# Optimization experiments

Hardware: AMD Instinct MI355X
Metric: run time of the kernel (lower is better)

Reference implementation:

```python
import jax, jax.numpy as jnp
import numpy as np

B, T, OBS = 256, 512, 256
H = 128          # OptimizedLSTMCell hidden size (hardcoded in module)
LATENT = 16


def setup_inputs() -> dict:
    key = jax.random.key(0)
    ks = jax.random.split(key, 6)
    xs = jax.random.normal(ks[0], (B, T, OBS), dtype=jnp.float32)
    # fused LSTM weights: gates ordered (i, f, g, o), each of width H
    Wx = jax.random.normal(ks[1], (OBS, 4 * H), dtype=jnp.float32) / np.sqrt(OBS)
    Wh = jax.random.normal(ks[2], (H, 4 * H), dtype=jnp.float32) / np.sqrt(H)
    b = jnp.zeros((4 * H,), dtype=jnp.float32)
    W1 = jax.random.normal(ks[3], (H, H), dtype=jnp.float32) / np.sqrt(H)
    b1 = jnp.zeros((H,), dtype=jnp.float32)
    W2 = jax.random.normal(ks[4], (H, 2 * LATENT), dtype=jnp.float32) / np.sqrt(H)
    b2 = jnp.zeros((2 * LATENT,), dtype=jnp.float32)
    return {"xs": xs, "Wx": Wx, "Wh": Wh, "b": b,
            "W1": W1, "b1": b1, "W2": W2, "b2": b2}


def reference(xs, Wx, Wh, b, W1, b1, W2, b2):
    # LSTM over time (flax OptimizedLSTMCell math, zero initial carry)
    bsz = xs.shape[0]
    hdim = Wh.shape[0]

    def step(carry, x_t):
        c, h = carry
        gates = x_t @ Wx + h @ Wh + b            # [B, 4H]
        i, f, g, o = jnp.split(gates, 4, axis=-1)
        i = jax.nn.sigmoid(i)
        f = jax.nn.sigmoid(f)
        g = jnp.tanh(g)
        o = jax.nn.sigmoid(o)
        c = f * c + i * g
        h = o * jnp.tanh(c)
        return (c, h), None

    init = (jnp.zeros((bsz, hdim), xs.dtype), jnp.zeros((bsz, hdim), xs.dtype))
    (_, h_last), _ = jax.lax.scan(step, init, jnp.swapaxes(xs, 0, 1))

    out = jax.nn.relu(h_last @ W1 + b1)          # [B, H]
    p = out @ W2 + b2                            # [B, 2*latent]
    mean, logvar = jnp.split(p, 2, axis=-1)
    return mean, logvar
```

## Files before the change

### kernel.cpp

```cpp
#include <hip/hip_runtime.h>
#include <hip/hip_fp16.h>

typedef unsigned short u16;
typedef unsigned int u32;

#define B_   256
#define T_   512
#define OBS_ 256
#define H_   128
#define G4_  512
#define LAT_ 16

typedef _Float16 half8_t __attribute__((ext_vector_type(8)));
typedef _Float16 half2_t __attribute__((ext_vector_type(2)));
typedef float    f32x4_t __attribute__((ext_vector_type(4)));

#if defined(__has_builtin)
#if __has_builtin(__builtin_amdgcn_fdot2)
#define HAVE_FDOT2 1
#endif
#endif

__device__ __forceinline__ u16 f2h(float x) { return __half_as_ushort(__float2half(x)); }
__device__ __forceinline__ float h2f(u16 u) { return __half2float(__ushort_as_half(u)); }
__device__ __forceinline__ float frcp(float x) { return __builtin_amdgcn_rcpf(x); }
__device__ __forceinline__ float fsigmoid(float x) { return frcp(1.f + __expf(-x)); }
__device__ __forceinline__ float ftanh(float x) { return 1.f - 2.f * frcp(1.f + __expf(2.f * x)); }

__device__ __forceinline__ float dot2acc(u32 w, u32 h, float acc) {
  half2_t wv = __builtin_bit_cast(half2_t, w);
  half2_t hv = __builtin_bit_cast(half2_t, h);
#ifdef HAVE_FDOT2
  return __builtin_amdgcn_fdot2(wv, hv, acc, false);
#else
  acc = fmaf((float)wv.x, (float)hv.x, acc);
  acc = fmaf((float)wv.y, (float)hv.y, acc);
  return acc;
#endif
}

__device__ __forceinline__ int permcol(int n) { return (n & 3) * 128 + (n >> 2); }

__global__ __launch_bounds__(256) void prep_kernel(const float* __restrict__ Wx,
                                                   const float* __restrict__ Wh,
                                                   const float* __restrict__ bias,
                                                   u16* __restrict__ Wxt,
                                                   u32* __restrict__ Whp,
                                                   float* __restrict__ biasp) {
  int idx = blockIdx.x * 256 + threadIdx.x;
  if (idx < G4_ * OBS_) {
    int n = idx / OBS_, k = idx % OBS_;
    Wxt[idx] = f2h(Wx[(size_t)k * G4_ + permcol(n)]);
  } else if (idx < G4_ * OBS_ + (H_ / 2) * G4_) {
    int i2 = idx - G4_ * OBS_;
    int k2 = i2 / G4_, n = i2 % G4_;
    int pn = permcol(n);
    u32 lo = f2h(Wh[(size_t)(2 * k2) * G4_ + pn]);
    u32 hi = f2h(Wh[(size_t)(2 * k2 + 1) * G4_ + pn]);
    Whp[i2] = lo | (hi << 16);
  } else if (idx < G4_ * OBS_ + (H_ / 2) * G4_ + G4_) {
    int n = idx - G4_ * OBS_ - (H_ / 2) * G4_;
    biasp[n] = bias[permcol(n)];
  }
}

__global__ __launch_bounds__(256, 2) void gemm_xw(const float* __restrict__ xs,
                                                  const u16* __restrict__ Wxt,
                                                  u16* __restrict__ Xw,
                                                  int t0, int ct_log2) {
  __shared__ __align__(16) u16 As[128][88];
  __shared__ __align__(16) u16 Bs[128][88];

  const int tid  = threadIdx.x;
  const int lane = tid & 63;
  const int w    = tid >> 6;
  const int qr   = (w & 1) * 64;
  const int qc   = (w >> 1) * 64;
  const int bn   = blockIdx.x;
  const int bm   = blockIdx.y;

  f32x4_t acc[4][4];
#pragma unroll
  for (int a = 0; a < 4; ++a)
#pragma unroll
    for (int bq = 0; bq < 4; ++bq)
      acc[a][bq] = (f32x4_t){0.f, 0.f, 0.f, 0.f};

  const int row  = tid >> 1;
  const int half = (tid & 1) * 32;
  const int m    = bm * 128 + row;
  const int bb   = m >> ct_log2;
  const int tau  = m & ((1 << ct_log2) - 1);
  const float* asrc = xs + (size_t)(bb * T_ + t0 + tau) * OBS_ + half;
  const u16*   bsrc = Wxt + (size_t)(bn * 128 + row) * OBS_ + half;

  for (int k0 = 0; k0 < OBS_; k0 += 64) {
    {
      const float* s = asrc + k0;
#pragma unroll
      for (int i = 0; i < 4; ++i) {
        float4 v0 = *(const float4*)(s + i * 8);
        float4 v1 = *(const float4*)(s + i * 8 + 4);
        uint4 pk;
        pk.x = (u32)f2h(v0.x) | ((u32)f2h(v0.y) << 16);
        pk.y = (u32)f2h(v0.z) | ((u32)f2h(v0.w) << 16);
        pk.z = (u32)f2h(v1.x) | ((u32)f2h(v1.y) << 16);
        pk.w = (u32)f2h(v1.z) | ((u32)f2h(v1.w) << 16);
        *(uint4*)&As[row][half + i * 8] = pk;
      }
    }
    {
      const u16* s = bsrc + k0;
#pragma unroll
      for (int i = 0; i < 4; ++i)
        *(uint4*)&Bs[row][half + i * 8] = *(const uint4*)(s + i * 8);
    }
    __syncthreads();
#pragma unroll
    for (int ks = 0; ks < 2; ++ks) {
      const int kc = ks * 32 + (lane >> 4) * 8;
      half8_t af[4], bf[4];
#pragma unroll
      for (int mi = 0; mi < 4; ++mi) af[mi] = *(const half8_t*)&As[qr + mi * 16 + (lane & 15)][kc];
#pragma unroll
      for (int ni = 0; ni < 4; ++ni) bf[ni] = *(const half8_t*)&Bs[qc + ni * 16 + (lane & 15)][kc];
#pragma unroll
      for (int mi = 0; mi < 4; ++mi)
#pragma unroll
        for (int ni = 0; ni < 4; ++ni)
          acc[mi][ni] = __builtin_amdgcn_mfma_f32_16x16x32_f16(af[mi], bf[ni], acc[mi][ni], 0, 0, 0);
    }
    __syncthreads();
  }
#pragma unroll
  for (int mi = 0; mi < 4; ++mi)
#pragma unroll
    for (int ni = 0; ni < 4; ++ni)
#pragma unroll
      for (int r = 0; r < 4; ++r) {
        int mm = bm * 128 + qr + mi * 16 + (lane >> 4) * 4 + r;
        int nn = bn * 128 + qc + ni * 16 + (lane & 15);
        Xw[(size_t)mm * G4_ + nn] = f2h(acc[mi][ni][r]);
      }
}

__global__ __launch_bounds__(512, 1) void lstm_rec(const u16* __restrict__ Xw,
                                                   const u32* __restrict__ Whp,
                                                   const float* __restrict__ biasp,
                                                   float* __restrict__ c_ws,
                                                   u16* __restrict__ h_ws,
                                                   int t0, int CT) {
  const int bb = blockIdx.x;
  const int tn = threadIdx.x;
  const int q  = tn & 3;
  const int j  = tn >> 2;
  __shared__ uint4 hq[2][16];

  u32 wh[64];
#pragma unroll
  for (int k2 = 0; k2 < 64; ++k2) wh[k2] = Whp[k2 * 512 + tn];
#pragma unroll
  for (int k2 = 0; k2 < 64; ++k2) asm volatile("" : "+v"(wh[k2]));
  const float bj = biasp[tn];

  float c = 0.f;
  if (t0 == 0) {
    if (tn < 32) ((uint4*)hq)[tn] = make_uint4(0u, 0u, 0u, 0u);
  } else {
    if (tn < 128) ((u16*)hq[0])[tn] = h_ws[bb * 128 + tn];
    if (q == 0) c = c_ws[bb * 128 + j];
  }
  __syncthreads();

  const u16* xwp = Xw + (size_t)bb * CT * 512 + tn;

  auto step = [&](u16 xcur, int cur) {
    float a0 = 0.f, a1 = 0.f, a2 = 0.f, a3 = 0.f;
#pragma unroll
    for (int qq = 0; qq < 16; ++qq) {
      uint4 hv = hq[cur][qq];
      a0 = dot2acc(wh[4 * qq + 0], hv.x, a0);
      a1 = dot2acc(wh[4 * qq + 1], hv.y, a1);
      a2 = dot2acc(wh[4 * qq + 2], hv.z, a2);
      a3 = dot2acc(wh[4 * qq + 3], hv.w, a3);
    }
    float pre = ((a0 + a1) + (a2 + a3)) + bj + h2f(xcur);
    float s1 = __shfl_xor(pre, 1);
    float s2 = __shfl_xor(pre, 2);
    float s3 = __shfl_xor(s1, 2);
    if (q == 0) {
      float ig = fsigmoid(pre);
      float fg = fsigmoid(s1);
      float gg = ftanh(s2);
      float og = fsigmoid(s3);
      c = fg * c + ig * gg;
      ((u16*)hq[cur ^ 1])[j] = f2h(og * ftanh(c));
    }
    __syncthreads();
  };

  u16 x0 = xwp[0 * 512], x1 = xwp[1 * 512], x2 = xwp[2 * 512], x3 = xwp[3 * 512];
  for (int t = 0; t < CT; t += 4) {
    u16 n0 = 0, n1 = 0, n2 = 0, n3 = 0;
    if (t + 4 < CT) {
      n0 = xwp[(size_t)(t + 4) * 512];
      n1 = xwp[(size_t)(t + 5) * 512];
      n2 = xwp[(size_t)(t + 6) * 512];
      n3 = xwp[(size_t)(t + 7) * 512];
    }
    step(x0, 0);
    step(x1, 1);
    step(x2, 0);
    step(x3, 1);
    x0 = n0; x1 = n1; x2 = n2; x3 = n3;
  }
  if (q == 0) {
    c_ws[bb * 128 + j] = c;
    h_ws[bb * 128 + j] = ((u16*)hq[0])[j];
  }
}

__global__ __launch_bounds__(128) void head_kernel(const u16* __restrict__ h_ws,
                                                   const float* __restrict__ W1,
                                                   const float* __restrict__ b1,
                                                   const float* __restrict__ W2,
                                                   const float* __restrict__ b2,
                                                   float* __restrict__ out) {
  const int bb = blockIdx.x;
  const int j  = threadIdx.x;
  __shared__ float hs[128];
  __shared__ float o1[128];
  hs[j] = h2f(h_ws[bb * 128 + j]);
  __syncthreads();
  float acc = b1[j];
#pragma unroll 8
  for (int k = 0; k < 128; ++k) acc = fmaf(hs[k], W1[(size_t)k * 128 + j], acc);
  o1[j] = fmaxf(acc, 0.f);
  __syncthreads();
  if (j < 2 * LAT_) {
    float acc2 = b2[j];
#pragma unroll 8
    for (int k = 0; k < 128; ++k) acc2 = fmaf(o1[k], W2[(size_t)k * (2 * LAT_) + j], acc2);
    if (j < LAT_) out[(size_t)bb * LAT_ + j] = acc2;
    else          out[(size_t)B_ * LAT_ + (size_t)bb * LAT_ + (j - LAT_)] = acc2;
  }
}

extern "C" void kernel_launch(void* const* d_in, const int* in_sizes, int n_in,
                              void* d_out, int out_size, void* d_ws, size_t ws_size,
                              hipStream_t stream) {
  const float* xs   = (const float*)d_in[0];
  const float* Wx   = (const float*)d_in[1];
  const float* Wh   = (const float*)d_in[2];
  const float* bias = (const float*)d_in[3];
  const float* W1   = (const float*)d_in[4];
  const float* b1   = (const float*)d_in[5];
  const float* W2   = (const float*)d_in[6];
  const float* b2   = (const float*)d_in[7];
  float* out = (float*)d_out;

  char* ws = (char*)d_ws;
  u16* Wxt    = (u16*)(ws + 0);
  u32* Whp    = (u32*)(ws + 262144);
  float* c_ws = (float*)(ws + 393216);
  u16* h_ws   = (u16*)(ws + 524288);
  float* biasp= (float*)(ws + 589824);
  u16* Xw     = (u16*)(ws + 591872);

  int CT = 512;
  while (CT > 128 && 591872 + (size_t)262144 * CT > ws_size) CT >>= 1;
  int ctl = __builtin_ctz((unsigned)CT);

  prep_kernel<<<642, 256, 0, stream>>>(Wx, Wh, bias, Wxt, Whp, biasp);
  for (int t0 = 0; t0 < T_; t0 += CT) {
    gemm_xw<<<dim3(4, 2 * CT), 256, 0, stream>>>(xs, Wxt, Xw, t0, ctl);
    lstm_rec<<<256, 512, 0, stream>>>(Xw, Whp, biasp, c_ws, h_ws, t0, CT);
  }
  head_kernel<<<256, 128, 0, stream>>>(h_ws, W1, b1, W2, b2, out);
}
```

Baseline: 441.5 us.

## Split LSTM recurrent dot product across two threads per gate column

The recurrent kernel now runs 1024 threads per block. Each pair of threads splits the 128-element hidden dot product for one gate column into halves, and a shuffle combines the two partial sums. This halves the per-thread serial dot chain and the weight registers on the latency-bound sequential path. In exchange it adds an extra shuffle per step and makes the per-step barrier span twice as many waves. The launch bound of 4 blocks of 1024 may be unreachable or may cap registers.

```diff
diff --git a/kernel.cpp b/kernel.cpp
--- a/kernel.cpp
+++ b/kernel.cpp
@@ -144,57 +144,58 @@
       }
 }
 
-__global__ __launch_bounds__(512, 1) void lstm_rec(const u16* __restrict__ Xw,
-                                                   const u32* __restrict__ Whp,
-                                                   const float* __restrict__ biasp,
-                                                   float* __restrict__ c_ws,
-                                                   u16* __restrict__ h_ws,
-                                                   int t0, int CT) {
+__global__ __launch_bounds__(1024, 4) void lstm_rec(const u16* __restrict__ Xw,
+                                                    const u32* __restrict__ Whp,
+                                                    const float* __restrict__ biasp,
+                                                    float* __restrict__ c_ws,
+                                                    u16* __restrict__ h_ws,
+                                                    int t0, int CT) {
   const int bb = blockIdx.x;
   const int tn = threadIdx.x;
-  const int q  = tn & 3;
-  const int j  = tn >> 2;
+  const int n  = tn >> 1;
+  const int kh = tn & 1;
+  const int q  = (tn >> 1) & 3;
   __shared__ uint4 hq[2][16];
 
-  u32 wh[64];
-#pragma unroll
-  for (int k2 = 0; k2 < 64; ++k2) wh[k2] = Whp[k2 * 512 + tn];
-#pragma unroll
-  for (int k2 = 0; k2 < 64; ++k2) asm volatile("" : "+v"(wh[k2]));
-  const float bj = biasp[tn];
+  u32 wh[32];
+#pragma unroll
+  for (int r = 0; r < 32; ++r) wh[r] = Whp[(kh * 32 + r) * 512 + n];
+  const float bj = biasp[n];
 
   float c = 0.f;
   if (t0 == 0) {
     if (tn < 32) ((uint4*)hq)[tn] = make_uint4(0u, 0u, 0u, 0u);
   } else {
     if (tn < 128) ((u16*)hq[0])[tn] = h_ws[bb * 128 + tn];
-    if (q == 0) c = c_ws[bb * 128 + j];
+    if ((tn & 7) == 0) c = c_ws[bb * 128 + (tn >> 3)];
   }
   __syncthreads();
 
-  const u16* xwp = Xw + (size_t)bb * CT * 512 + tn;
+  const u16* xwp = Xw + (size_t)bb * CT * 512 + n;
+  const int kh8 = kh * 8;
 
   auto step = [&](u16 xcur, int cur) {
     float a0 = 0.f, a1 = 0.f, a2 = 0.f, a3 = 0.f;
 #pragma unroll
-    for (int qq = 0; qq < 16; ++qq) {
-      uint4 hv = hq[cur][qq];
+    for (int qq = 0; qq < 8; ++qq) {
+      uint4 hv = hq[cur][kh8 + qq];
       a0 = dot2acc(wh[4 * qq + 0], hv.x, a0);
       a1 = dot2acc(wh[4 * qq + 1], hv.y, a1);
       a2 = dot2acc(wh[4 * qq + 2], hv.z, a2);
       a3 = dot2acc(wh[4 * qq + 3], hv.w, a3);
     }
-    float pre = ((a0 + a1) + (a2 + a3)) + bj + h2f(xcur);
-    float s1 = __shfl_xor(pre, 1);
-    float s2 = __shfl_xor(pre, 2);
-    float s3 = __shfl_xor(s1, 2);
-    if (q == 0) {
+    float part = (a0 + a1) + (a2 + a3);
+    float pre = part + __shfl_xor(part, 1) + bj + h2f(xcur);
+    float s1 = __shfl_xor(pre, 2);
+    float s2 = __shfl_xor(pre, 4);
+    float s3 = __shfl_xor(s1, 4);
+    if ((tn & 7) == 0) {
       float ig = fsigmoid(pre);
       float fg = fsigmoid(s1);
       float gg = ftanh(s2);
       float og = fsigmoid(s3);
       c = fg * c + ig * gg;
-      ((u16*)hq[cur ^ 1])[j] = f2h(og * ftanh(c));
+      ((u16*)hq[cur ^ 1])[tn >> 3] = f2h(og * ftanh(c));
     }
     __syncthreads();
   };
@@ -214,9 +215,9 @@
     step(x3, 1);
     x0 = n0; x1 = n1; x2 = n2; x3 = n3;
   }
-  if (q == 0) {
-    c_ws[bb * 128 + j] = c;
-    h_ws[bb * 128 + j] = ((u16*)hq[0])[j];
+  if ((tn & 7) == 0) {
+    c_ws[bb * 128 + (tn >> 3)] = c;
+    h_ws[bb * 128 + (tn >> 3)] = ((u16*)hq[0])[tn >> 3];
   }
 }
 
@@ -274,7 +275,7 @@
   prep_kernel<<<642, 256, 0, stream>>>(Wx, Wh, bias, Wxt, Whp, biasp);
   for (int t0 = 0; t0 < T_; t0 += CT) {
     gemm_xw<<<dim3(4, 2 * CT), 256, 0, stream>>>(xs, Wxt, Xw, t0, ctl);
-    lstm_rec<<<256, 512, 0, stream>>>(Xw, Whp, biasp, c_ws, h_ws, t0, CT);
+    lstm_rec<<<256, 1024, 0, stream>>>(Xw, Whp, biasp, c_ws, h_ws, t0, CT);
   }
   head_kernel<<<256, 128, 0, stream>>>(h_ws, W1, b1, W2, b2, out);
 }
```

Result: slower. 545.9 us (+23.6%).

## Split LSTM recurrence over K with shuffle reduction instead of gate-per-thread

Applied to the files above, without the earlier changes.

Recasts the per-step recurrent matvec so that each group of four threads splits the hidden dimension into quarters and computes all four gates of one hidden unit, reducing the partial sums with xor shuffles. Previously each thread owned a single gate column over the full K and gate values were exchanged by shuffles. Weights are now loaded as dwordx4 through inline asm, and the input projection is read as one uint2 per step. Every lane now evaluates the nonlinearities redundantly, which removes the q==0 divergence. The loop is no longer unrolled by four, and the launch-bounds hint changes to waves_per_eu(2,2).

```diff
diff --git a/kernel.cpp b/kernel.cpp
--- a/kernel.cpp
+++ b/kernel.cpp
@@ -144,79 +144,83 @@
       }
 }
 
-__global__ __launch_bounds__(512, 1) void lstm_rec(const u16* __restrict__ Xw,
-                                                   const u32* __restrict__ Whp,
-                                                   const float* __restrict__ biasp,
-                                                   float* __restrict__ c_ws,
-                                                   u16* __restrict__ h_ws,
-                                                   int t0, int CT) {
-  const int bb = blockIdx.x;
-  const int tn = threadIdx.x;
-  const int q  = tn & 3;
-  const int j  = tn >> 2;
-  __shared__ uint4 hq[2][16];
-
-  u32 wh[64];
-#pragma unroll
-  for (int k2 = 0; k2 < 64; ++k2) wh[k2] = Whp[k2 * 512 + tn];
-#pragma unroll
-  for (int k2 = 0; k2 < 64; ++k2) asm volatile("" : "+v"(wh[k2]));
-  const float bj = biasp[tn];
+__global__ __launch_bounds__(512) __attribute__((amdgpu_waves_per_eu(2, 2)))
+void lstm_rec(const u16* __restrict__ Xw,
+              const u32* __restrict__ Whp,
+              const float* __restrict__ biasp,
+              float* __restrict__ c_ws,
+              u16* __restrict__ h_ws,
+              int t0, int CT) {
+  const int bb  = blockIdx.x;
+  const int tid = threadIdx.x;
+  const int s   = tid & 3;
+  const int j   = tid >> 2;
+  __shared__ u32 hq[2][64];
+
+  uint4 W[16];
+  {
+    const u32* base = Whp + (size_t)(16 * s) * 512 + 4 * j;
+#pragma unroll
+    for (int r = 0; r < 16; ++r)
+      asm volatile("global_load_dwordx4 %0, %1, off"
+                   : "=v"(W[r]) : "v"(base + (size_t)r * 512));
+    asm volatile("s_waitcnt vmcnt(0)" ::: "memory");
+  }
+  const float4 bj = *(const float4*)(biasp + 4 * j);
 
   float c = 0.f;
   if (t0 == 0) {
-    if (tn < 32) ((uint4*)hq)[tn] = make_uint4(0u, 0u, 0u, 0u);
+    if (tid < 64) hq[0][tid] = 0u;
   } else {
-    if (tn < 128) ((u16*)hq[0])[tn] = h_ws[bb * 128 + tn];
-    if (q == 0) c = c_ws[bb * 128 + j];
+    if (tid < 64) hq[0][tid] = ((const u32*)h_ws)[bb * 64 + tid];
+    c = c_ws[bb * 128 + j];
   }
   __syncthreads();
 
-  const u16* xwp = Xw + (size_t)bb * CT * 512 + tn;
-
-  auto step = [&](u16 xcur, int cur) {
-    float a0 = 0.f, a1 = 0.f, a2 = 0.f, a3 = 0.f;
-#pragma unroll
-    for (int qq = 0; qq < 16; ++qq) {
-      uint4 hv = hq[cur][qq];
-      a0 = dot2acc(wh[4 * qq + 0], hv.x, a0);
-      a1 = dot2acc(wh[4 * qq + 1], hv.y, a1);
-      a2 = dot2acc(wh[4 * qq + 2], hv.z, a2);
-      a3 = dot2acc(wh[4 * qq + 3], hv.w, a3);
-    }
-    float pre = ((a0 + a1) + (a2 + a3)) + bj + h2f(xcur);
-    float s1 = __shfl_xor(pre, 1);
-    float s2 = __shfl_xor(pre, 2);
-    float s3 = __shfl_xor(s1, 2);
-    if (q == 0) {
-      float ig = fsigmoid(pre);
-      float fg = fsigmoid(s1);
-      float gg = ftanh(s2);
-      float og = fsigmoid(s3);
-      c = fg * c + ig * gg;
-      ((u16*)hq[cur ^ 1])[j] = f2h(og * ftanh(c));
-    }
+  const u16* xwrow = Xw + (size_t)bb * CT * 512 + 4 * j;
+  uint2 xw = *(const uint2*)(xwrow);
+  float hval = 0.f;
+
+  for (int t = 0; t < CT; ++t) {
+    uint2 xwn = make_uint2(0u, 0u);
+    if (t + 1 < CT) xwn = *(const uint2*)(xwrow + (size_t)(t + 1) * 512);
+
+    const u32* hp = &hq[t & 1][16 * s];
+    uint4 h0 = *(const uint4*)(hp);
+    uint4 h1 = *(const uint4*)(hp + 4);
+    uint4 h2 = *(const uint4*)(hp + 8);
+    uint4 h3 = *(const uint4*)(hp + 12);
+    u32 hv[16] = {h0.x, h0.y, h0.z, h0.w, h1.x, h1.y, h1.z, h1.w,
+                  h2.x, h2.y, h2.z, h2.w, h3.x, h3.y, h3.z, h3.w};
+
+    float p0 = 0.f, p1 = 0.f, p2 = 0.f, p3 = 0.f;
+#pragma unroll
+    for (int r = 0; r < 16; ++r) {
+      p0 = dot2acc(W[r].x, hv[r], p0);
+      p1 = dot2acc(W[r].y, hv[r], p1);
+      p2 = dot2acc(W[r].z, hv[r], p2);
+      p3 = dot2acc(W[r].w, hv[r], p3);
+    }
+    p0 += __shfl_xor(p0, 1); p0 += __shfl_xor(p0, 2);
+    p1 += __shfl_xor(p1, 1); p1 += __shfl_xor(p1, 2);
+    p2 += __shfl_xor(p2, 1); p2 += __shfl_xor(p2, 2);
+    p3 += __shfl_xor(p3, 1); p3 += __shfl_xor(p3, 2);
+
+    half2_t xlo = __builtin_bit_cast(half2_t, xw.x);
+    half2_t xhi = __builtin_bit_cast(half2_t, xw.y);
+    float ig = fsigmoid(p0 + bj.x + (float)xlo.x);
+    float fg = fsigmoid(p1 + bj.y + (float)xlo.y);
+    float gg = ftanh   (p2 + bj.z + (float)xhi.x);
+    float og = fsigmoid(p3 + bj.w + (float)xhi.y);
+    c = fg * c + ig * gg;
+    hval = og * ftanh(c);
+    if (s == 0) ((u16*)&hq[(t + 1) & 1][0])[j] = f2h(hval);
     __syncthreads();
-  };
-
-  u16 x0 = xwp[0 * 512], x1 = xwp[1 * 512], x2 = xwp[2 * 512], x3 = xwp[3 * 512];
-  for (int t = 0; t < CT; t += 4) {
-    u16 n0 = 0, n1 = 0, n2 = 0, n3 = 0;
-    if (t + 4 < CT) {
-      n0 = xwp[(size_t)(t + 4) * 512];
-      n1 = xwp[(size_t)(t + 5) * 512];
-      n2 = xwp[(size_t)(t + 6) * 512];
-      n3 = xwp[(size_t)(t + 7) * 512];
-    }
-    step(x0, 0);
-    step(x1, 1);
-    step(x2, 0);
-    step(x3, 1);
-    x0 = n0; x1 = n1; x2 = n2; x3 = n3;
-  }
-  if (q == 0) {
+    xw = xwn;
+  }
+  if (s == 0) {
     c_ws[bb * 128 + j] = c;
-    h_ws[bb * 128 + j] = ((u16*)hq[0])[j];
+    h_ws[bb * 128 + j] = f2h(hval);
   }
 }
 
```

Result: slower. 481.6 us (+9.1%).
